# Performance work log

Hardware: AMD Instinct MI355X
Metric: run time of the kernel (lower is better)

Reference implementation:

```python
import jax, jax.numpy as jnp
import numpy as np

EPS = 1e-10
MARGIN = 0.05
DELTA = 0.1
H = W = 512
N = 8388608


def setup_inputs() -> dict:
    key = jax.random.key(0)
    k1, k2, k3, k4 = jax.random.split(key, 4)
    v_input = jax.random.uniform(k1, (3, H, W), dtype=jnp.float32)
    coords = jax.random.randint(k2, (N, 4), 0, W, dtype=jnp.int32)  # x1,y1,x2,y2
    darker = jax.random.randint(k3, (N,), 0, 3, dtype=jnp.int32)
    weights = jax.random.uniform(k4, (N,), dtype=jnp.float32)
    return {"v_input": v_input, "coords": coords, "darker": darker, "weights": weights}


def reference(v_input, coords, darker, weights):
    # v = sum over channels / 3, then affine remap (exactly as torch code)
    v = jnp.sum(v_input, axis=0) / 3.0
    v = (v * 255.0 + 1.0) / 256.0  # [H, W]

    x1, y1, x2, y2 = coords[:, 0], coords[:, 1], coords[:, 2], coords[:, 3]
    r1 = v[y1, x1]
    r2 = v[y2, x2]
    ratio = r1 / (r2 + EPS)
    ratio_inv = r2 / (r1 + EPS)

    b = 1.0 + DELTA + MARGIN
    inv_b = 1.0 / b
    # darker == 1: penalize if ratio > 1/b
    l1 = jnp.where(ratio > inv_b, (ratio - inv_b) + (b - ratio_inv), 0.0)
    # darker == 2: penalize if ratio < b
    l2 = jnp.where(ratio < b, (b - ratio) + (ratio_inv - inv_b), 0.0)
    # darker == 0 (margin <= delta branch): two-sided hinge around [bl, br]
    br = 1.0 + DELTA - MARGIN
    bl = 1.0 / br
    l0 = jnp.where(
        ratio > br,
        (ratio - br) + (bl - ratio_inv),
        jnp.where(ratio < bl, (bl - ratio) + (ratio_inv - br), 0.0),
    )

    per = jnp.where(darker == 1, l1, jnp.where(darker == 2, l2, l0))
    loss = jnp.sum(weights * per) / np.float32(coords.shape[0])
    return loss
```

## Files before the change

kernel.cpp:

```cpp
#include <hip/hip_runtime.h>

#define HW 512
#define NPIX (HW * HW)
#define LDS_PIX 163840
#define K 16
#define THREADS 1024
#define BLOCKS 512

#define EPS_F  1e-10f
constexpr double B_d  = 1.0 + 0.1 + 0.05;
constexpr double BR_d = 1.0 + 0.1 - 0.05;
#define B_F    ((float)B_d)
#define INVB_F ((float)(1.0 / B_d))
#define BR_F   ((float)BR_d)
#define BL_F   ((float)(1.0 / BR_d))

typedef __attribute__((ext_vector_type(4))) int ivec4;

__global__ void build_v(const float* __restrict__ vin,
                        unsigned char* __restrict__ vq,
                        float* __restrict__ out) {
    int i = blockIdx.x * blockDim.x + threadIdx.x;
    if (i == 0) *out = 0.0f;
    if (i < NPIX) {
        float s = vin[i] + vin[i + NPIX] + vin[i + 2 * NPIX];
        float m = s * (1.0f / 3.0f);
        vq[i] = (unsigned char)__float2int_rn(m * 255.0f);
    }
}

__device__ __forceinline__ float per_loss(float r1, float r2, int d) {
    float ratio = r1 / (r2 + EPS_F);
    float rinv  = r2 / (r1 + EPS_F);
    float l1 = (ratio > INVB_F) ? (ratio - INVB_F + (B_F - rinv)) : 0.0f;
    float l2 = (ratio < B_F)    ? (B_F - ratio + (rinv - INVB_F)) : 0.0f;
    float l0 = (ratio > BR_F)   ? (ratio - BR_F + (BL_F - rinv))
             : ((ratio < BL_F)  ? (BL_F - ratio + (rinv - BR_F)) : 0.0f);
    return (d == 1) ? l1 : ((d == 2) ? l2 : l0);
}

__global__ __launch_bounds__(THREADS) void whdr_kernel(
        const unsigned char* __restrict__ vq,
        const ivec4* __restrict__ coords,
        const int*   __restrict__ darker,
        const float* __restrict__ weights,
        float*       __restrict__ out,
        int n) {
    __shared__ unsigned char lv[LDS_PIX];
    {
        const uint4* s4 = (const uint4*)vq;
        uint4* d4 = (uint4*)lv;
        #pragma unroll
        for (int j = threadIdx.x; j < LDS_PIX / 16; j += THREADS) d4[j] = s4[j];
    }
    __syncthreads();

    const int tid = blockIdx.x * THREADS + threadIdx.x;
    const int T   = gridDim.x * THREADS;
    float acc = 0.0f;

    if (tid + (K - 1) * T < n) {
        ivec4 c[K];
        #pragma unroll
        for (int k = 0; k < K; ++k) c[k] = __builtin_nontemporal_load(&coords[tid + k * T]);
        int i1[K], i2[K];
        #pragma unroll
        for (int k = 0; k < K; ++k) { i1[k] = c[k].y * HW + c[k].x; i2[k] = c[k].w * HW + c[k].z; }
        unsigned q1[K], q2[K];
        #pragma unroll
        for (int k = 0; k < K; ++k) {
            if (i1[k] < LDS_PIX) q1[k] = lv[i1[k]]; else q1[k] = vq[i1[k]];
            if (i2[k] < LDS_PIX) q2[k] = lv[i2[k]]; else q2[k] = vq[i2[k]];
        }
        int   dk[K];
        float w[K];
        #pragma unroll
        for (int k = 0; k < K; ++k) dk[k] = __builtin_nontemporal_load(&darker[tid + k * T]);
        #pragma unroll
        for (int k = 0; k < K; ++k) w[k]  = __builtin_nontemporal_load(&weights[tid + k * T]);
        __builtin_amdgcn_sched_barrier(0);
        #pragma unroll
        for (int k = 0; k < K; ++k) {
            float r1 = (float)(q1[k] + 1) * (1.0f / 256.0f);
            float r2 = (float)(q2[k] + 1) * (1.0f / 256.0f);
            acc += w[k] * per_loss(r1, r2, dk[k]);
        }
    } else {
        for (int i = tid; i < n; i += T) {
            ivec4 c = coords[i];
            float a = (float)(vq[c.y * HW + c.x] + 1) * (1.0f / 256.0f);
            float b = (float)(vq[c.w * HW + c.z] + 1) * (1.0f / 256.0f);
            acc += weights[i] * per_loss(a, b, darker[i]);
        }
    }

    #pragma unroll
    for (int off = 32; off > 0; off >>= 1)
        acc += __shfl_down(acc, off, 64);
    __syncthreads();
    float* wsum = (float*)lv;
    int lane = threadIdx.x & 63;
    int wid  = threadIdx.x >> 6;
    if (lane == 0) wsum[wid] = acc;
    __syncthreads();
    if (threadIdx.x == 0) {
        float s = 0.0f;
        #pragma unroll
        for (int i = 0; i < THREADS / 64; ++i) s += wsum[i];
        atomicAdd(out, s * (1.0f / 8388608.0f));
    }
}

extern "C" void kernel_launch(void* const* d_in, const int* in_sizes, int n_in,
                              void* d_out, int out_size, void* d_ws, size_t ws_size,
                              hipStream_t stream) {
    const float* v_input = (const float*)d_in[0];
    const ivec4* coords  = (const ivec4*)d_in[1];
    const int*   darker  = (const int*)d_in[2];
    const float* weights = (const float*)d_in[3];
    float* out = (float*)d_out;
    unsigned char* vq = (unsigned char*)d_ws;
    int n = in_sizes[2];

    build_v<<<(NPIX + 255) / 256, 256, 0, stream>>>(v_input, vq, out);
    whdr_kernel<<<BLOCKS, THREADS, 0, stream>>>(vq, coords, darker, weights, out, n);
}
```

Baseline: 250.8 us.

## Software-pipeline streamed loads in rounds and overlap them with LDS table fill

The single 16-deep batch of loads is split into four rounds of four elements, with two register sets double-buffered so the next round's coords, darker and weights are prefetched while the current round is computed. The first two rounds' loads are issued before the LDS copy of the quantized table, so that global latency overlaps the table fill and barrier. The divisions become hardware reciprocal multiplies. The trade-off is less exact division, a fast path that only applies when n equals grid size times 16, and a fallback loop that now also reads from LDS.

```diff
diff --git a/kernel.cpp b/kernel.cpp
--- a/kernel.cpp
+++ b/kernel.cpp
@@ -3,9 +3,10 @@
 #define HW 512
 #define NPIX (HW * HW)
 #define LDS_PIX 163840
-#define K 16
 #define THREADS 1024
 #define BLOCKS 512
+#define NB 4
+#define RNDS 4
 
 #define EPS_F  1e-10f
 constexpr double B_d  = 1.0 + 0.1 + 0.05;
@@ -29,14 +30,65 @@
     }
 }
 
+__device__ __forceinline__ float rcp_fast(float x) {
+#if __has_builtin(__builtin_amdgcn_rcpf)
+    return __builtin_amdgcn_rcpf(x);
+#else
+    return 1.0f / x;
+#endif
+}
+
 __device__ __forceinline__ float per_loss(float r1, float r2, int d) {
-    float ratio = r1 / (r2 + EPS_F);
-    float rinv  = r2 / (r1 + EPS_F);
+    float ratio = r1 * rcp_fast(r2 + EPS_F);
+    float rinv  = r2 * rcp_fast(r1 + EPS_F);
     float l1 = (ratio > INVB_F) ? (ratio - INVB_F + (B_F - rinv)) : 0.0f;
     float l2 = (ratio < B_F)    ? (B_F - ratio + (rinv - INVB_F)) : 0.0f;
     float l0 = (ratio > BR_F)   ? (ratio - BR_F + (BL_F - rinv))
              : ((ratio < BL_F)  ? (BL_F - ratio + (rinv - BR_F)) : 0.0f);
     return (d == 1) ? l1 : ((d == 2) ? l2 : l0);
+}
+
+template<bool PF>
+__device__ __forceinline__ void do_round(
+        ivec4 (&cc)[NB], int (&dd)[NB], float (&ww)[NB],
+        const unsigned char* lv, const unsigned char* __restrict__ vq,
+        const ivec4* __restrict__ coords, const int* __restrict__ darker,
+        const float* __restrict__ weights,
+        int tid, int T, int pfofs, float& acc)
+{
+    int i1[NB], i2[NB];
+    unsigned q1[NB], q2[NB];
+    #pragma unroll
+    for (int k = 0; k < NB; ++k) {
+        i1[k] = cc[k].y * HW + cc[k].x;
+        i2[k] = cc[k].w * HW + cc[k].z;
+    }
+    #pragma unroll
+    for (int k = 0; k < NB; ++k) {
+        q1[k] = (i1[k] < LDS_PIX) ? (unsigned)lv[i1[k]] : (unsigned)vq[i1[k]];
+        q2[k] = (i2[k] < LDS_PIX) ? (unsigned)lv[i2[k]] : (unsigned)vq[i2[k]];
+    }
+    if (PF) {
+        #pragma unroll
+        for (int k = 0; k < NB; ++k)
+            cc[k] = __builtin_nontemporal_load(&coords[tid + (pfofs + k) * T]);
+    }
+    __builtin_amdgcn_sched_barrier(0);
+    #pragma unroll
+    for (int k = 0; k < NB; ++k) {
+        float r1 = (float)(q1[k] + 1) * (1.0f / 256.0f);
+        float r2 = (float)(q2[k] + 1) * (1.0f / 256.0f);
+        acc += ww[k] * per_loss(r1, r2, dd[k]);
+    }
+    if (PF) {
+        #pragma unroll
+        for (int k = 0; k < NB; ++k)
+            dd[k] = __builtin_nontemporal_load(&darker[tid + (pfofs + k) * T]);
+        #pragma unroll
+        for (int k = 0; k < NB; ++k)
+            ww[k] = __builtin_nontemporal_load(&weights[tid + (pfofs + k) * T]);
+        __builtin_amdgcn_sched_barrier(0);
+    }
 }
 
 __global__ __launch_bounds__(THREADS) void whdr_kernel(
@@ -47,50 +99,54 @@
         float*       __restrict__ out,
         int n) {
     __shared__ unsigned char lv[LDS_PIX];
-    {
-        const uint4* s4 = (const uint4*)vq;
-        uint4* d4 = (uint4*)lv;
-        #pragma unroll
-        for (int j = threadIdx.x; j < LDS_PIX / 16; j += THREADS) d4[j] = s4[j];
-    }
-    __syncthreads();
-
     const int tid = blockIdx.x * THREADS + threadIdx.x;
-    const int T   = gridDim.x * THREADS;
+    const int T   = BLOCKS * THREADS;
     float acc = 0.0f;
 
-    if (tid + (K - 1) * T < n) {
-        ivec4 c[K];
+    if (n == T * NB * RNDS) {
+        ivec4 cA[NB], cB[NB];
+        int   dA[NB], dB[NB];
+        float wA[NB], wB[NB];
         #pragma unroll
-        for (int k = 0; k < K; ++k) c[k] = __builtin_nontemporal_load(&coords[tid + k * T]);
-        int i1[K], i2[K];
+        for (int k = 0; k < NB; ++k) cA[k] = __builtin_nontemporal_load(&coords[tid + k * T]);
         #pragma unroll
-        for (int k = 0; k < K; ++k) { i1[k] = c[k].y * HW + c[k].x; i2[k] = c[k].w * HW + c[k].z; }
-        unsigned q1[K], q2[K];
+        for (int k = 0; k < NB; ++k) dA[k] = __builtin_nontemporal_load(&darker[tid + k * T]);
         #pragma unroll
-        for (int k = 0; k < K; ++k) {
-            if (i1[k] < LDS_PIX) q1[k] = lv[i1[k]]; else q1[k] = vq[i1[k]];
-            if (i2[k] < LDS_PIX) q2[k] = lv[i2[k]]; else q2[k] = vq[i2[k]];
+        for (int k = 0; k < NB; ++k) wA[k] = __builtin_nontemporal_load(&weights[tid + k * T]);
+        #pragma unroll
+        for (int k = 0; k < NB; ++k) cB[k] = __builtin_nontemporal_load(&coords[tid + (NB + k) * T]);
+        #pragma unroll
+        for (int k = 0; k < NB; ++k) dB[k] = __builtin_nontemporal_load(&darker[tid + (NB + k) * T]);
+        #pragma unroll
+        for (int k = 0; k < NB; ++k) wB[k] = __builtin_nontemporal_load(&weights[tid + (NB + k) * T]);
+        {
+            const uint4* s4 = (const uint4*)vq;
+            uint4* d4 = (uint4*)lv;
+            #pragma unroll
+            for (int j = threadIdx.x; j < LDS_PIX / 16; j += THREADS) d4[j] = s4[j];
         }
-        int   dk[K];
-        float w[K];
-        #pragma unroll
-        for (int k = 0; k < K; ++k) dk[k] = __builtin_nontemporal_load(&darker[tid + k * T]);
-        #pragma unroll
-        for (int k = 0; k < K; ++k) w[k]  = __builtin_nontemporal_load(&weights[tid + k * T]);
-        __builtin_amdgcn_sched_barrier(0);
-        #pragma unroll
-        for (int k = 0; k < K; ++k) {
-            float r1 = (float)(q1[k] + 1) * (1.0f / 256.0f);
-            float r2 = (float)(q2[k] + 1) * (1.0f / 256.0f);
-            acc += w[k] * per_loss(r1, r2, dk[k]);
+        __syncthreads();
+
+        do_round<true >(cA, dA, wA, lv, vq, coords, darker, weights, tid, T, 2 * NB, acc);
+        do_round<true >(cB, dB, wB, lv, vq, coords, darker, weights, tid, T, 3 * NB, acc);
+        do_round<false>(cA, dA, wA, lv, vq, coords, darker, weights, tid, T, 0, acc);
+        do_round<false>(cB, dB, wB, lv, vq, coords, darker, weights, tid, T, 0, acc);
+    } else {
+        {
+            const uint4* s4 = (const uint4*)vq;
+            uint4* d4 = (uint4*)lv;
+            for (int j = threadIdx.x; j < LDS_PIX / 16; j += THREADS) d4[j] = s4[j];
         }
-    } else {
-        for (int i = tid; i < n; i += T) {
+        __syncthreads();
+        const int TT = gridDim.x * THREADS;
+        for (int i = tid; i < n; i += TT) {
             ivec4 c = coords[i];
-            float a = (float)(vq[c.y * HW + c.x] + 1) * (1.0f / 256.0f);
-            float b = (float)(vq[c.w * HW + c.z] + 1) * (1.0f / 256.0f);
-            acc += weights[i] * per_loss(a, b, darker[i]);
+            int i1 = c.y * HW + c.x, i2 = c.w * HW + c.z;
+            unsigned a = (i1 < LDS_PIX) ? (unsigned)lv[i1] : (unsigned)vq[i1];
+            unsigned b = (i2 < LDS_PIX) ? (unsigned)lv[i2] : (unsigned)vq[i2];
+            float r1 = (float)(a + 1) * (1.0f / 256.0f);
+            float r2 = (float)(b + 1) * (1.0f / 256.0f);
+            acc += weights[i] * per_loss(r1, r2, darker[i]);
         }
     }
 
@@ -107,7 +163,7 @@
         float s = 0.0f;
         #pragma unroll
         for (int i = 0; i < THREADS / 64; ++i) s += wsum[i];
-        atomicAdd(out, s * (1.0f / 8388608.0f));
+        atomicAdd(out, s / (float)n);
     }
 }
 
```

New measurement: 249.8 us. About the same (-0.4%).
